# Optimization experiments

Measured on AMD Instinct MI355X. Metric: run time of the kernel, lower is better.

The kernel has to match this reference:

```python
import jax, jax.numpy as jnp
import numpy as np

N, E, H, D, F_IN = 50000, 400000, 2, 128, 5
EPS = 1e-5  # BatchNorm eps

def _bn(x, gamma, beta, rm, rv):
    # eval-mode BatchNorm1d using running stats
    return (x - rm) * jax.lax.rsqrt(rv + EPS) * gamma + beta

def setup_inputs() -> dict:
    key = jax.random.key(0)
    ks = jax.random.split(key, 24)
    r = lambda i, shape, s=1.0: jax.random.normal(ks[i], shape, jnp.float32) * s
    u = lambda i, shape: jax.random.uniform(ks[i], shape, jnp.float32)
    return {
        "h": r(0, (N, F_IN)),
        "edge_index": jax.random.randint(ks[1], (2, E), 0, N),
        "edge_weight": r(2, (E, 1)),
        # BatchNorm1d(5)
        "gamma1": 1.0 + r(3, (F_IN,), 0.1), "beta1": r(4, (F_IN,), 0.1),
        "rm1": r(5, (F_IN,), 0.1), "rv1": 0.5 + u(6, (F_IN,)),
        # GATv2Conv params (lin_l, lin_r with bias; lin_edge no bias; att; out bias)
        "Wl": r(7, (F_IN, H * D), 0.2), "bl": r(8, (H * D,), 0.1),
        "Wr": r(9, (F_IN, H * D), 0.2), "br": r(10, (H * D,), 0.1),
        "We": r(11, (1, H * D), 0.2),
        "att": r(12, (H, D), 0.2),
        "bias_gat": r(13, (D,), 0.1),
        # fc1 + BatchNorm1d(128)
        "W1": r(14, (D, D), 0.08), "b1": r(15, (D,), 0.1),
        "gamma2": 1.0 + r(16, (D,), 0.1), "beta2": r(17, (D,), 0.1),
        "rm2": r(18, (D,), 0.1), "rv2": 0.5 + u(19, (D,)),
        # fc2
        "W2": r(20, (D, F_IN), 0.08), "b2": r(21, (F_IN,), 0.1),
    }

def reference(h, edge_index, edge_weight, gamma1, beta1, rm1, rv1,
              Wl, bl, Wr, br, We, att, bias_gat,
              W1, b1, gamma2, beta2, rm2, rv2, W2, b2):
    src, dst = edge_index[0], edge_index[1]
    h = _bn(h, gamma1, beta1, rm1, rv1)
    xl = (h @ Wl + bl).reshape(N, H, D)   # source transform (messages)
    xr = (h @ Wr + br).reshape(N, H, D)   # destination transform
    e = (edge_weight @ We).reshape(E, H, D)
    # GATv2: score = att . leaky_relu(x_j + x_i + edge_emb), slope 0.2
    z = jax.nn.leaky_relu(xl[src] + xr[dst] + e, 0.2)          # [E,H,D]
    logits = jnp.einsum('ehd,hd->eh', z, att)                   # [E,H]
    # segment softmax over edges sharing a destination node
    mx = jax.ops.segment_max(logits, dst, num_segments=N)       # [N,H]
    ex = jnp.exp(logits - mx[dst])
    den = jax.ops.segment_sum(ex, dst, num_segments=N)
    alpha = ex / (den[dst] + 1e-16)                             # [E,H]
    msg = xl[src] * alpha[:, :, None]                           # [E,H,D]
    ssum = jax.ops.segment_sum(msg, dst, num_segments=N)        # [N,H,D]
    cnt = jax.ops.segment_sum(jnp.ones((E,), jnp.float32), dst, num_segments=N)
    out = ssum / jnp.maximum(cnt, 1.0)[:, None, None]           # aggr='mean'
    out = out.mean(axis=1) + bias_gat                           # concat=False -> head mean
    out = out @ W1 + b1
    out = _bn(out, gamma2, beta2, rm2, rv2)
    out = jax.nn.leaky_relu(out, 0.01)
    # dropout is identity in eval mode
    out = out @ W2 + b2                                         # [N,5]
    return out
```

## Files before the change

### kernel.cpp

```cpp
#include <hip/hip_runtime.h>

#define N_NODES 50000
#define N_EDGES 400000
#define F_INP 5
#define HD 256
#define BN_EPS 1e-5f

typedef short v8s __attribute__((ext_vector_type(8)));
typedef float v4f __attribute__((ext_vector_type(4)));
typedef unsigned v4u __attribute__((ext_vector_type(4)));

#define OFF_HBN  0
#define OFF_ACC  400000
#define OFF_BPK  1200000
#define OFF_WF   1204096
#define OFF_W2P  1206144

#define PREP_BLOCKS 3125
#define NT_ALL   25000

#define DPP_ROR_F(x, n) \
    __int_as_float(__builtin_amdgcn_update_dpp(0, __float_as_int(x), 0x120 | (n), 0xF, 0xF, false))

__device__ __forceinline__ unsigned short f2bf(float f) {
    unsigned u = __float_as_uint(f);
    return (unsigned short)((u + 0x7FFFu + ((u >> 16) & 1u)) >> 16);
}
__device__ __forceinline__ unsigned pk2(float a, float b) {
    return (unsigned)f2bf(a) | ((unsigned)f2bf(b) << 16);
}

__device__ __forceinline__ float wcat(int k, int c, const float* Wl, const float* Wr,
                                      const float* We, const float* bl, const float* br) {
    if (k < 5)   return Wl[k * HD + c];
    if (k < 10)  return Wr[(k - 5) * HD + c];
    if (k == 10) return We[c];
    return bl[c] + br[c];
}

__global__ void k_prep(const float* __restrict__ h, const float* __restrict__ g1,
                       const float* __restrict__ be1, const float* __restrict__ rm1,
                       const float* __restrict__ rv1,
                       const float* __restrict__ Wl, const float* __restrict__ bl,
                       const float* __restrict__ Wr, const float* __restrict__ br,
                       const float* __restrict__ We, const float* __restrict__ att,
                       const float* __restrict__ bias_gat,
                       const float* __restrict__ W1, const float* __restrict__ b1,
                       const float* __restrict__ g2, const float* __restrict__ be2,
                       const float* __restrict__ rm2, const float* __restrict__ rv2,
                       const float* __restrict__ W2,
                       float* __restrict__ hbn8, float* __restrict__ acc,
                       uint4* __restrict__ Bq,
                       float* __restrict__ Wf, float* __restrict__ W2p) {
    if (blockIdx.x < PREP_BLOCKS) {
        int i = blockIdx.x * blockDim.x + threadIdx.x;
        if (i < N_NODES * 16) acc[i] = 0.f;
        if (i < N_NODES * 8) {
            int f = i & 7, n = i >> 3;
            float v = 0.f;
            if (f < F_INP) {
                float x = h[n * F_INP + f];
                v = (x - rm1[f]) * rsqrtf(rv1[f] + BN_EPS) * g1[f] + be1[f];
            }
            hbn8[i] = v;
        }
        if (i < 1024) {
            int t = i >> 6, l = i & 63;
            int g = l >> 4, c = t * 16 + (l & 15);
            unsigned d0 = 0, d1 = 0;
            if (g < 3) {
                int kb = 4 * g;
                d0 = pk2(wcat(kb + 0, c, Wl, Wr, We, bl, br),
                         wcat(kb + 1, c, Wl, Wr, We, bl, br));
                d1 = pk2(wcat(kb + 2, c, Wl, Wr, We, bl, br),
                         wcat(kb + 3, c, Wl, Wr, We, bl, br));
            }
            Bq[i] = make_uint4(d0, d1, __float_as_uint(att[c]), 0u);
        }
        return;
    }
    int k = blockIdx.x - PREP_BLOCKS;
    int c = threadIdx.x;
    if (c >= 128) return;
    const float* base = (k == 0) ? bl
                      : (k == 1) ? bl + 128
                      : (k < 7)  ? Wl + (k - 2) * HD
                      : (k < 12) ? Wl + (k - 7) * HD + 128
                                 : bias_gat;
    float sum = 0.f;
#pragma unroll 8
    for (int d = 0; d < 128; ++d) sum += base[d] * W1[d * 128 + c];
    if (k == 12) sum += b1[c];
    Wf[c * 16 + k] = sum;
    if (k == 0) {
        float sc = g2[c] * rsqrtf(rv2[c] + BN_EPS);
        Wf[c * 16 + 13] = sc;
        Wf[c * 16 + 14] = be2[c] - rm2[c] * sc;
        Wf[c * 16 + 15] = 0.f;
#pragma unroll
        for (int f = 0; f < 8; ++f)
            W2p[c * 8 + f] = (f < 5) ? W2[c * 5 + f] : 0.f;
    }
}

__launch_bounds__(256)
__global__ void k_edge(const float* __restrict__ hbn8, const int* __restrict__ ei,
                       const float* __restrict__ ew, const uint4* __restrict__ Bq,
                       float* __restrict__ acc) {
    __shared__ uint4 Bsh[1024];
    for (int i = threadIdx.x; i < 1024; i += 256) Bsh[i] = Bq[i];
    __syncthreads();

    int lane = threadIdx.x & 63;
    int wv = threadIdx.x >> 6;
    int g = lane >> 4, e16 = lane & 15;

    int wid = blockIdx.x * 4 + wv;
    int nw = gridDim.x * 4;

    int j16 = e16;
    bool sact = j16 < 13;
    int kk = (j16 < 6) ? j16 - 1 : j16 - 7;
    int kc = min(max(kk, 0), 4);

    for (int tile = wid; tile < NT_ALL; tile += nw) {
        int e = tile * 16 + e16;
        int src = ei[e];
        int dst = ei[N_EDGES + e];
        float w = ew[e];
        float4 s4 = *(const float4*)&hbn8[src * 8];
        float hs4 = hbn8[src * 8 + 4];
        float4 d4 = *(const float4*)&hbn8[dst * 8];
        float hd4 = hbn8[dst * 8 + 4];

        float a0 = (g == 0) ? s4.x : (g == 1) ? hs4  : d4.w;
        float a1 = (g == 0) ? s4.y : (g == 1) ? d4.x : hd4;
        float a2 = (g == 0) ? s4.z : (g == 1) ? d4.y : w;
        float a3 = (g == 0) ? s4.w : (g == 1) ? d4.z : 1.0f;
        unsigned ua0 = (g < 3) ? pk2(a0, a1) : 0u;
        unsigned ua1 = (g < 3) ? pk2(a2, a3) : 0u;
        v4u uav = {ua0, ua1, 0u, 0u};
        v8s A = __builtin_bit_cast(v8s, uav);

        float p00 = 0.f, p01 = 0.f, p02 = 0.f, p03 = 0.f;
        float p10 = 0.f, p11 = 0.f, p12 = 0.f, p13v = 0.f;
        v4f zero = {0.f, 0.f, 0.f, 0.f};
#pragma unroll
        for (int t = 0; t < 8; ++t) {
            uint4 bb = Bsh[t * 64 + lane];
            v4u u = {bb.x, bb.y, 0u, 0u};
            v8s Bt = __builtin_bit_cast(v8s, u);
            float ATt = __uint_as_float(bb.z);
            v4f c = __builtin_amdgcn_mfma_f32_16x16x32_bf16(A, Bt, zero, 0, 0, 0);
            p00 += ATt * fmaf(0.66666667f, fabsf(c[0]), c[0]);
            p01 += ATt * fmaf(0.66666667f, fabsf(c[1]), c[1]);
            p02 += ATt * fmaf(0.66666667f, fabsf(c[2]), c[2]);
            p03 += ATt * fmaf(0.66666667f, fabsf(c[3]), c[3]);
        }
#pragma unroll
        for (int t = 8; t < 16; ++t) {
            uint4 bb = Bsh[t * 64 + lane];
            v4u u = {bb.x, bb.y, 0u, 0u};
            v8s Bt = __builtin_bit_cast(v8s, u);
            float ATt = __uint_as_float(bb.z);
            v4f c = __builtin_amdgcn_mfma_f32_16x16x32_bf16(A, Bt, zero, 0, 0, 0);
            p10 += ATt * fmaf(0.66666667f, fabsf(c[0]), c[0]);
            p11 += ATt * fmaf(0.66666667f, fabsf(c[1]), c[1]);
            p12 += ATt * fmaf(0.66666667f, fabsf(c[2]), c[2]);
            p13v += ATt * fmaf(0.66666667f, fabsf(c[3]), c[3]);
        }
        p00 += DPP_ROR_F(p00, 1); p01 += DPP_ROR_F(p01, 1);
        p02 += DPP_ROR_F(p02, 1); p03 += DPP_ROR_F(p03, 1);
        p10 += DPP_ROR_F(p10, 1); p11 += DPP_ROR_F(p11, 1);
        p12 += DPP_ROR_F(p12, 1); p13v += DPP_ROR_F(p13v, 1);
        p00 += DPP_ROR_F(p00, 2); p01 += DPP_ROR_F(p01, 2);
        p02 += DPP_ROR_F(p02, 2); p03 += DPP_ROR_F(p03, 2);
        p10 += DPP_ROR_F(p10, 2); p11 += DPP_ROR_F(p11, 2);
        p12 += DPP_ROR_F(p12, 2); p13v += DPP_ROR_F(p13v, 2);
        p00 += DPP_ROR_F(p00, 4); p01 += DPP_ROR_F(p01, 4);
        p02 += DPP_ROR_F(p02, 4); p03 += DPP_ROR_F(p03, 4);
        p10 += DPP_ROR_F(p10, 4); p11 += DPP_ROR_F(p11, 4);
        p12 += DPP_ROR_F(p12, 4); p13v += DPP_ROR_F(p13v, 4);
        p00 += DPP_ROR_F(p00, 8); p01 += DPP_ROR_F(p01, 8);
        p02 += DPP_ROR_F(p02, 8); p03 += DPP_ROR_F(p03, 8);
        p10 += DPP_ROR_F(p10, 8); p11 += DPP_ROR_F(p11, 8);
        p12 += DPP_ROR_F(p12, 8); p13v += DPP_ROR_F(p13v, 8);

        float e00 = __expf(0.6f * p00), e01 = __expf(0.6f * p01);
        float e02 = __expf(0.6f * p02), e03 = __expf(0.6f * p03);
        float e10 = __expf(0.6f * p10), e11 = __expf(0.6f * p11);
        float e12 = __expf(0.6f * p12), e13 = __expf(0.6f * p13v);

        if (sact) {
#pragma unroll
            for (int it = 0; it < 4; ++it) {
                int eg = tile * 16 + 4 * g + it;
                int srcg = ei[eg];
                int deg = ei[N_EDGES + eg];
                float hsel = hbn8[srcg * 8 + kc];
                float ex0 = (it == 0) ? e00 : (it == 1) ? e01 : (it == 2) ? e02 : e03;
                float ex1 = (it == 0) ? e10 : (it == 1) ? e11 : (it == 2) ? e12 : e13;
                float base = (j16 < 6) ? ex0 : ex1;
                float v = base * hsel;
                v = (j16 == 0) ? ex0 : v;
                v = (j16 == 6) ? ex1 : v;
                v = (j16 == 12) ? 1.0f : v;
                atomicAdd(&acc[deg * 16 + j16], v);
            }
        }
    }
}

__launch_bounds__(256)
__global__ void k_mlp(const float* __restrict__ acc, const float* __restrict__ Wf,
                      const float* __restrict__ W2p, const float* __restrict__ b2,
                      float* __restrict__ out) {
    int n = blockIdx.x * blockDim.x + threadIdx.x;
    if (n >= N_NODES) return;
    const float* ar = acc + (size_t)n * 16;
    float4 A0 = *(const float4*)(ar + 0);
    float4 A1 = *(const float4*)(ar + 4);
    float4 A2 = *(const float4*)(ar + 8);
    float cnt = ar[12];
    float r0 = 1.f / (A0.x + 1e-16f);
    float r1 = 1.f / (A1.z + 1e-16f);
    float scale = 0.5f / fmaxf(cnt, 1.f);
    float s0 = scale * r0, s1 = scale * r1;
    float m0 = A0.x * s0, m1 = A1.z * s1;
    float m2 = A0.y * s0, m3 = A0.z * s0, m4 = A0.w * s0, m5 = A1.x * s0, m6 = A1.y * s0;
    float m7 = A1.w * s1, m8 = A2.x * s1, m9 = A2.y * s1, m10 = A2.z * s1, m11 = A2.w * s1;

    float o0 = 0.f, o1 = 0.f, o2 = 0.f, o3 = 0.f, o4 = 0.f;
#pragma unroll 4
    for (int c = 0; c < 128; ++c) {
        const float* wr = &Wf[c * 16];
        float a = wr[12];
        a += m0 * wr[0] + m1 * wr[1] + m2 * wr[2] + m3 * wr[3];
        a += m4 * wr[4] + m5 * wr[5] + m6 * wr[6] + m7 * wr[7];
        a += m8 * wr[8] + m9 * wr[9] + m10 * wr[10] + m11 * wr[11];
        a = fmaf(a, wr[13], wr[14]);
        a = fmaxf(a, 0.01f * a);
        const float* w2 = &W2p[c * 8];
        o0 = fmaf(a, w2[0], o0);
        o1 = fmaf(a, w2[1], o1);
        o2 = fmaf(a, w2[2], o2);
        o3 = fmaf(a, w2[3], o3);
        o4 = fmaf(a, w2[4], o4);
    }
    float* op = out + (size_t)n * 5;
    op[0] = o0 + b2[0];
    op[1] = o1 + b2[1];
    op[2] = o2 + b2[2];
    op[3] = o3 + b2[3];
    op[4] = o4 + b2[4];
}

extern "C" void kernel_launch(void* const* d_in, const int* in_sizes, int n_in,
                              void* d_out, int out_size, void* d_ws, size_t ws_size,
                              hipStream_t stream) {
    const float* h    = (const float*)d_in[0];
    const int*   ei   = (const int*)d_in[1];
    const float* ew   = (const float*)d_in[2];
    const float* g1   = (const float*)d_in[3];
    const float* be1  = (const float*)d_in[4];
    const float* rm1  = (const float*)d_in[5];
    const float* rv1  = (const float*)d_in[6];
    const float* Wl   = (const float*)d_in[7];
    const float* bl   = (const float*)d_in[8];
    const float* Wr   = (const float*)d_in[9];
    const float* br   = (const float*)d_in[10];
    const float* We   = (const float*)d_in[11];
    const float* att  = (const float*)d_in[12];
    const float* bias_gat = (const float*)d_in[13];
    const float* W1   = (const float*)d_in[14];
    const float* b1   = (const float*)d_in[15];
    const float* g2   = (const float*)d_in[16];
    const float* be2  = (const float*)d_in[17];
    const float* rm2  = (const float*)d_in[18];
    const float* rv2  = (const float*)d_in[19];
    const float* W2   = (const float*)d_in[20];
    const float* b2   = (const float*)d_in[21];

    float* ws  = (float*)d_ws;
    float* hbn = ws + OFF_HBN;
    float* acc = ws + OFF_ACC;
    uint4* Bq  = (uint4*)(ws + OFF_BPK);
    float* Wf  = ws + OFF_WF;
    float* W2p = ws + OFF_W2P;

    k_prep<<<PREP_BLOCKS + 13, 256, 0, stream>>>(
        h, g1, be1, rm1, rv1, Wl, bl, Wr, br, We, att, bias_gat,
        W1, b1, g2, be2, rm2, rv2, W2, hbn, acc, Bq, Wf, W2p);
    k_edge<<<2048, 256, 0, stream>>>(hbn, ei, ew, Bq, acc);
    k_mlp<<<(N_NODES + 255) / 256, 256, 0, stream>>>(acc, Wf, W2p, b2, (float*)d_out);
}
```

Baseline: 88.86 us.

## Split edge kernel into logit computation and separate atomic scatter kernel

```diff
diff --git a/kernel.cpp b/kernel.cpp
--- a/kernel.cpp
+++ b/kernel.cpp
@@ -15,9 +15,11 @@
 #define OFF_BPK  1200000
 #define OFF_WF   1204096
 #define OFF_W2P  1206144
+#define OFF_EXB  1207168
 
 #define PREP_BLOCKS 3125
 #define NT_ALL   25000
+#define NQ_ALL   100000
 
 #define DPP_ROR_F(x, n) \
     __int_as_float(__builtin_amdgcn_update_dpp(0, __float_as_int(x), 0x120 | (n), 0xF, 0xF, false))
@@ -103,10 +105,10 @@
     }
 }
 
-__launch_bounds__(256)
-__global__ void k_edge(const float* __restrict__ hbn8, const int* __restrict__ ei,
-                       const float* __restrict__ ew, const uint4* __restrict__ Bq,
-                       float* __restrict__ acc) {
+__launch_bounds__(256, 4)
+__global__ void k_logit(const float* __restrict__ hbn8, const int* __restrict__ ei,
+                        const float* __restrict__ ew, const uint4* __restrict__ Bq,
+                        float* __restrict__ exb) {
     __shared__ uint4 Bsh[1024];
     for (int i = threadIdx.x; i < 1024; i += 256) Bsh[i] = Bq[i];
     __syncthreads();
@@ -114,14 +116,11 @@
     int lane = threadIdx.x & 63;
     int wv = threadIdx.x >> 6;
     int g = lane >> 4, e16 = lane & 15;
+    int r4 = lane & 3;
+    bool wr_act = (lane & 12) == 0;
 
     int wid = blockIdx.x * 4 + wv;
     int nw = gridDim.x * 4;
-
-    int j16 = e16;
-    bool sact = j16 < 13;
-    int kk = (j16 < 6) ? j16 - 1 : j16 - 7;
-    int kc = min(max(kk, 0), 4);
 
     for (int tile = wid; tile < NT_ALL; tile += nw) {
         int e = tile * 16 + e16;
@@ -186,27 +185,45 @@
         p10 += DPP_ROR_F(p10, 8); p11 += DPP_ROR_F(p11, 8);
         p12 += DPP_ROR_F(p12, 8); p13v += DPP_ROR_F(p13v, 8);
 
-        float e00 = __expf(0.6f * p00), e01 = __expf(0.6f * p01);
-        float e02 = __expf(0.6f * p02), e03 = __expf(0.6f * p03);
-        float e10 = __expf(0.6f * p10), e11 = __expf(0.6f * p11);
-        float e12 = __expf(0.6f * p12), e13 = __expf(0.6f * p13v);
-
-        if (sact) {
-#pragma unroll
-            for (int it = 0; it < 4; ++it) {
-                int eg = tile * 16 + 4 * g + it;
-                int srcg = ei[eg];
-                int deg = ei[N_EDGES + eg];
-                float hsel = hbn8[srcg * 8 + kc];
-                float ex0 = (it == 0) ? e00 : (it == 1) ? e01 : (it == 2) ? e02 : e03;
-                float ex1 = (it == 0) ? e10 : (it == 1) ? e11 : (it == 2) ? e12 : e13;
-                float base = (j16 < 6) ? ex0 : ex1;
-                float v = base * hsel;
-                v = (j16 == 0) ? ex0 : v;
-                v = (j16 == 6) ? ex1 : v;
-                v = (j16 == 12) ? 1.0f : v;
-                atomicAdd(&acc[deg * 16 + j16], v);
-            }
+        if (wr_act) {
+            float w0 = (r4 == 0) ? p00 : (r4 == 1) ? p01 : (r4 == 2) ? p02 : p03;
+            float w1 = (r4 == 0) ? p10 : (r4 == 1) ? p11 : (r4 == 2) ? p12 : p13v;
+            int pos = 4 * g + r4;
+            exb[tile * 32 + pos]      = __expf(0.6f * w0);
+            exb[tile * 32 + 16 + pos] = __expf(0.6f * w1);
+        }
+    }
+}
+
+__launch_bounds__(256, 8)
+__global__ void k_scat(const float* __restrict__ hbn8, const int* __restrict__ ei,
+                       const float* __restrict__ exb, float* __restrict__ acc) {
+    int lane = threadIdx.x & 63;
+    int wv = threadIdx.x >> 6;
+    int q13 = lane / 13;
+    int j13 = lane - q13 * 13;
+    bool act = lane < 52;
+    int kk = (j13 < 6) ? j13 - 1 : j13 - 7;
+    int kc = min(max(kk, 0), 4);
+
+    int wid = blockIdx.x * 4 + wv;
+    int nw = gridDim.x * 4;
+
+    for (int q = wid; q < NQ_ALL; q += nw) {
+        if (act) {
+            int e = q * 4 + q13;
+            int src = ei[e];
+            int dst = ei[N_EDGES + e];
+            int tile = e >> 4, pos = e & 15;
+            float ex0 = exb[tile * 32 + pos];
+            float ex1 = exb[tile * 32 + 16 + pos];
+            float hsel = hbn8[src * 8 + kc];
+            float base = (j13 < 6) ? ex0 : ex1;
+            float v = base * hsel;
+            v = (j13 == 0) ? ex0 : v;
+            v = (j13 == 6) ? ex1 : v;
+            v = (j13 == 12) ? 1.0f : v;
+            atomicAdd(&acc[dst * 16 + j13], v);
         }
     }
 }
@@ -287,10 +304,12 @@
     uint4* Bq  = (uint4*)(ws + OFF_BPK);
     float* Wf  = ws + OFF_WF;
     float* W2p = ws + OFF_W2P;
+    float* exb = ws + OFF_EXB;
 
     k_prep<<<PREP_BLOCKS + 13, 256, 0, stream>>>(
         h, g1, be1, rm1, rv1, Wl, bl, Wr, br, We, att, bias_gat,
         W1, b1, g2, be2, rm2, rv2, W2, hbn, acc, Bq, Wf, W2p);
-    k_edge<<<2048, 256, 0, stream>>>(hbn, ei, ew, Bq, acc);
+    k_logit<<<2048, 256, 0, stream>>>(hbn, ei, ew, Bq, exb);
+    k_scat<<<2048, 256, 0, stream>>>(hbn, ei, exb, acc);
     k_mlp<<<(N_NODES + 255) / 256, 256, 0, stream>>>(acc, Wf, W2p, b2, (float*)d_out);
 }
```

After: 104.5 us. 1.18x slower.
